# Optimization experiments

Hardware: AMD Instinct MI355X
Metric: run time of the kernel (lower is better)

Reference implementation:

```python
import jax, jax.numpy as jnp
import numpy as np

B, S, H = 32, 2048, 1024

def setup_inputs() -> dict:
    key = jax.random.key(0)
    k1, k2, k3, k4, k5 = jax.random.split(key, 5)
    sc = 1.0 / np.sqrt(2 * H)
    return {
        "hidden": jax.random.normal(k1, (B, H), dtype=jnp.float32),
        "encoder_outputs": jax.random.normal(k2, (B, S, H), dtype=jnp.float32),
        "W_attn": jax.random.normal(k3, (2 * H, H), dtype=jnp.float32) * sc,
        "b_attn": jax.random.normal(k4, (H,), dtype=jnp.float32) * sc,
        "v": jax.random.normal(k5, (H,), dtype=jnp.float32) * (1.0 / np.sqrt(H)),
    }

def reference(hidden, encoder_outputs, W_attn, b_attn, v):
    # Split W_attn into hidden-part and encoder-part instead of materializing
    # the (B,S,2H) concat: cat([h, enc]) @ W == h @ W[:H] + enc @ W[H:]
    Wh, We = W_attn[:H], W_attn[H:]                       # (H,H) each
    h_proj = hidden @ Wh + b_attn                          # (B, H)
    e_proj = jnp.einsum('bsh,hk->bsk', encoder_outputs, We)  # (B, S, H)
    energy = jnp.tanh(h_proj[:, None, :] + e_proj)         # (B, S, H)
    attention = jnp.einsum('bsh,h->bs', energy, v)         # (B, S)
    return jax.nn.softmax(attention, axis=1)
```

## Files before the change

### kernel.cpp

```cpp
#include <hip/hip_runtime.h>
#include <hip/hip_bf16.h>

#define H 1024
#define SEQ 2048
#define BATCH 32
#define MTOT (BATCH * SEQ)

#define BM 128
#define BN 128
#define BK 64

typedef __attribute__((ext_vector_type(4))) float f32x4;
typedef __attribute__((ext_vector_type(8))) __bf16 bf16x8;
typedef __attribute__((ext_vector_type(8))) unsigned short ushort8;

__device__ __forceinline__ unsigned short f2bf(float x) {
  __hip_bfloat16 h = __float2bfloat16(x);
  return __builtin_bit_cast(unsigned short, h);
}

__device__ __forceinline__ void gload_lds16(const void* g, void* l) {
  __builtin_amdgcn_global_load_lds(
      (const __attribute__((address_space(1))) unsigned int*)g,
      (__attribute__((address_space(3))) unsigned int*)l, 16, 0, 0);
}

__global__ void we_transpose_kernel(const float* __restrict__ W,
                                    unsigned short* __restrict__ WeT) {
  __shared__ float t[64][65];
  const int bn = blockIdx.x * 64;
  const int bk = blockIdx.y * 64;
  const int tid = threadIdx.x;
  const int ln = tid & 63;
  const int lk = tid >> 6;
  const float* src = W + (size_t)(H + bk) * H + bn;
#pragma unroll
  for (int i = 0; i < 16; ++i) {
    int k = i * 4 + lk;
    t[k][ln] = src[(size_t)k * H + ln];
  }
  __syncthreads();
  const int n = tid >> 2;
  const int kg = tid & 3;
  ushort8 o0, o1;
#pragma unroll
  for (int j = 0; j < 8; ++j) o0[j] = f2bf(t[kg * 16 + j][n]);
#pragma unroll
  for (int j = 0; j < 8; ++j) o1[j] = f2bf(t[kg * 16 + 8 + j][n]);
  unsigned short* dst = WeT + (size_t)(bn + n) * H + bk + kg * 16;
  *(ushort8*)(dst) = o0;
  *(ushort8*)(dst + 8) = o1;
}

__global__ void hproj_kernel(const float* __restrict__ hidden,
                             const float* __restrict__ W,
                             const float* __restrict__ b_attn,
                             float* __restrict__ hproj) {
  __shared__ float h[H];
  const int b = blockIdx.y;
  const int n = blockIdx.x * 256 + threadIdx.x;
  for (int i = threadIdx.x; i < H; i += 256) h[i] = hidden[(size_t)b * H + i];
  __syncthreads();
  float acc = b_attn[n];
#pragma unroll 8
  for (int k = 0; k < H; ++k) acc = fmaf(h[k], W[(size_t)k * H + n], acc);
  hproj[(size_t)b * H + n] = acc;
}

__global__ __launch_bounds__(256) void gemm_fused_kernel(
    const float* __restrict__ A,
    const unsigned short* __restrict__ WeT,
    const float* __restrict__ hproj,
    const float* __restrict__ v,
    float* __restrict__ partials)
{
  __shared__ __align__(16) unsigned short As[BM * BK];
  __shared__ __align__(16) unsigned short Bs[BN * BK];
  __shared__ float red[2][BM];

  const int bid = blockIdx.x;
  const int nb = bid & 7;
  const int mt = bid >> 3;
  const int m0 = mt * BM;
  const int bb = m0 / SEQ;

  const int tid = threadIdx.x;
  const int lane = tid & 63;
  const int w = tid >> 6;
  const int wm = w >> 1;
  const int wn = w & 1;

  const int a_c = tid & 15;
  const int a_r0 = tid >> 4;
  const float* a_src = A + (size_t)(m0 + a_r0) * H + a_c * 4;
  char* AsB = (char*)As;
  char* BsB = (char*)Bs;

  const char* b_src[4];
  char* b_dst[4];
#pragma unroll
  for (int i = 0; i < 4; ++i) {
    int q = (w * 4 + i) * 64 + lane;
    int nl = q >> 3;
    int c = (q & 7) ^ (nl & 7);
    b_src[i] = (const char*)WeT + ((size_t)(nb * 128 + nl) * H + c * 8) * 2;
    b_dst[i] = BsB + (w * 4 + i) * 1024;
  }

  f32x4 acc[4][4] = {};

  for (int ks = 0; ks < H / BK; ++ks) {
#pragma unroll
    for (int i = 0; i < 4; ++i) gload_lds16(b_src[i] + ks * 128, b_dst[i]);
#pragma unroll
    for (int p = 0; p < 8; ++p) {
      const int row = a_r0 + p * 16;
      f32x4 f = *(const f32x4*)(a_src + (size_t)p * 16 * H + ks * 64);
      unsigned int lo = f2bf(f[0]) | ((unsigned int)f2bf(f[1]) << 16);
      unsigned int hi = f2bf(f[2]) | ((unsigned int)f2bf(f[3]) << 16);
      int boff = (row * 128 + a_c * 8) ^ ((row & 7) << 4);
      *(uint2*)(AsB + boff) = make_uint2(lo, hi);
    }
    __syncthreads();

    bf16x8 af[4][2], bfr[4][2];
#pragma unroll
    for (int mi = 0; mi < 4; ++mi)
#pragma unroll
      for (int kk = 0; kk < 2; ++kk) {
        int row = wm * 64 + mi * 16 + (lane & 15);
        int c = kk * 4 + (lane >> 4);
        int off = (row * 128 + c * 16) ^ ((row & 7) << 4);
        af[mi][kk] = *(const bf16x8*)(AsB + off);
      }
#pragma unroll
    for (int ni = 0; ni < 4; ++ni)
#pragma unroll
      for (int kk = 0; kk < 2; ++kk) {
        int nl = wn * 64 + ni * 16 + (lane & 15);
        int c = kk * 4 + (lane >> 4);
        int off = (nl * 128 + c * 16) ^ ((nl & 7) << 4);
        bfr[ni][kk] = *(const bf16x8*)(BsB + off);
      }
#pragma unroll
    for (int kk = 0; kk < 2; ++kk)
#pragma unroll
      for (int mi = 0; mi < 4; ++mi)
#pragma unroll
        for (int ni = 0; ni < 4; ++ni)
          acc[mi][ni] = __builtin_amdgcn_mfma_f32_16x16x32_bf16(
              af[mi][kk], bfr[ni][kk], acc[mi][ni], 0, 0, 0);
    __syncthreads();
  }

  float rowsum[4][4];
#pragma unroll
  for (int mi = 0; mi < 4; ++mi)
#pragma unroll
    for (int i = 0; i < 4; ++i) rowsum[mi][i] = 0.f;

  const int colb = nb * 128 + wn * 64;
#pragma unroll
  for (int ni = 0; ni < 4; ++ni) {
    int colg = colb + ni * 16 + (lane & 15);
    float hp = hproj[(size_t)bb * H + colg];
    float vv = v[colg];
#pragma unroll
    for (int mi = 0; mi < 4; ++mi)
#pragma unroll
      for (int i = 0; i < 4; ++i)
        rowsum[mi][i] += tanhf(acc[mi][ni][i] + hp) * vv;
  }
#pragma unroll
  for (int mask = 1; mask <= 8; mask <<= 1)
#pragma unroll
    for (int mi = 0; mi < 4; ++mi)
#pragma unroll
      for (int i = 0; i < 4; ++i)
        rowsum[mi][i] += __shfl_xor(rowsum[mi][i], mask, 64);

  if ((lane & 15) == 0) {
    int rg = lane >> 4;
#pragma unroll
    for (int mi = 0; mi < 4; ++mi)
#pragma unroll
      for (int i = 0; i < 4; ++i)
        red[wn][wm * 64 + mi * 16 + rg * 4 + i] = rowsum[mi][i];
  }
  __syncthreads();
  if (tid < BM)
    partials[(size_t)nb * MTOT + m0 + tid] = red[0][tid] + red[1][tid];
}

__global__ void softmax_kernel(const float* __restrict__ partials,
                               float* __restrict__ out) {
  const int b = blockIdx.x;
  const int tid = threadIdx.x;
  const int ln = tid & 63;
  const int wid = tid >> 6;
  __shared__ float r1[4], r2[4];
  float loc[8];
  float lmax = -3.4e38f;
#pragma unroll
  for (int j = 0; j < 8; ++j) {
    int s = j * 256 + tid;
    float acc = 0.f;
#pragma unroll
    for (int p = 0; p < 8; ++p)
      acc += partials[(size_t)p * MTOT + (size_t)b * SEQ + s];
    loc[j] = acc;
    lmax = fmaxf(lmax, acc);
  }
#pragma unroll
  for (int m = 1; m <= 32; m <<= 1) lmax = fmaxf(lmax, __shfl_xor(lmax, m, 64));
  if (ln == 0) r1[wid] = lmax;
  __syncthreads();
  const float gmax = fmaxf(fmaxf(r1[0], r1[1]), fmaxf(r1[2], r1[3]));
  float lsum = 0.f;
#pragma unroll
  for (int j = 0; j < 8; ++j) {
    loc[j] = expf(loc[j] - gmax);
    lsum += loc[j];
  }
#pragma unroll
  for (int m = 1; m <= 32; m <<= 1) lsum += __shfl_xor(lsum, m, 64);
  if (ln == 0) r2[wid] = lsum;
  __syncthreads();
  const float inv = 1.f / (r2[0] + r2[1] + r2[2] + r2[3]);
#pragma unroll
  for (int j = 0; j < 8; ++j)
    out[(size_t)b * SEQ + j * 256 + tid] = loc[j] * inv;
}

extern "C" void kernel_launch(void* const* d_in, const int* in_sizes, int n_in,
                              void* d_out, int out_size, void* d_ws, size_t ws_size,
                              hipStream_t stream) {
  const float* hidden = (const float*)d_in[0];
  const float* enc    = (const float*)d_in[1];
  const float* W      = (const float*)d_in[2];
  const float* b_attn = (const float*)d_in[3];
  const float* v      = (const float*)d_in[4];
  float* out = (float*)d_out;

  char* ws = (char*)d_ws;
  unsigned short* WeT = (unsigned short*)ws;
  float* hproj    = (float*)(ws + (2u << 20));
  float* partials = (float*)(ws + (2u << 20) + (128u << 10));

  we_transpose_kernel<<<dim3(16, 16), 256, 0, stream>>>(W, WeT);
  hproj_kernel<<<dim3(4, BATCH), 256, 0, stream>>>(hidden, W, b_attn, hproj);
  gemm_fused_kernel<<<dim3(4096), 256, 0, stream>>>(enc, WeT, hproj, v, partials);
  softmax_kernel<<<dim3(BATCH), 256, 0, stream>>>(partials, out);
}
```

Measured before the change: 695.4 us.

## Double-buffer GEMM LDS tiles with register prefetch and remap blocks per XCD

```diff
diff --git a/kernel.cpp b/kernel.cpp
--- a/kernel.cpp
+++ b/kernel.cpp
@@ -9,6 +9,8 @@
 #define BM 128
 #define BN 128
 #define BK 64
+#define KSTEPS (H / BK)
+#define BUFB (BM * BK * 2)
 
 typedef __attribute__((ext_vector_type(4))) float f32x4;
 typedef __attribute__((ext_vector_type(8))) __bf16 bf16x8;
@@ -74,13 +76,15 @@
     const float* __restrict__ v,
     float* __restrict__ partials)
 {
-  __shared__ __align__(16) unsigned short As[BM * BK];
-  __shared__ __align__(16) unsigned short Bs[BN * BK];
+  __shared__ __align__(16) unsigned short As[2][BM * BK];
+  __shared__ __align__(16) unsigned short Bs[2][BN * BK];
   __shared__ float red[2][BM];
 
-  const int bid = blockIdx.x;
-  const int nb = bid & 7;
-  const int mt = bid >> 3;
+  const int d = blockIdx.x;
+  const int x = d & 7;
+  const int ii = d >> 3;
+  const int nb = ii & 7;
+  const int mt = x * 64 + (ii >> 3);
   const int m0 = mt * BM;
   const int bb = m0 / SEQ;
 
@@ -95,33 +99,50 @@
   const float* a_src = A + (size_t)(m0 + a_r0) * H + a_c * 4;
   char* AsB = (char*)As;
   char* BsB = (char*)Bs;
-
-  const char* b_src[4];
-  char* b_dst[4];
+  const int a_boff = (a_r0 * 128 + a_c * 8) ^ ((a_r0 & 7) << 4);
+
+  const char* bsrc[4];
+  int bdst[4];
 #pragma unroll
   for (int i = 0; i < 4; ++i) {
     int q = (w * 4 + i) * 64 + lane;
     int nl = q >> 3;
     int c = (q & 7) ^ (nl & 7);
-    b_src[i] = (const char*)WeT + ((size_t)(nb * 128 + nl) * H + c * 8) * 2;
-    b_dst[i] = BsB + (w * 4 + i) * 1024;
+    bsrc[i] = (const char*)WeT + ((size_t)(nb * 128 + nl) * H + c * 8) * 2;
+    bdst[i] = (w * 4 + i) * 1024;
   }
 
   f32x4 acc[4][4] = {};
 
-  for (int ks = 0; ks < H / BK; ++ks) {
-#pragma unroll
-    for (int i = 0; i < 4; ++i) gload_lds16(b_src[i] + ks * 128, b_dst[i]);
-#pragma unroll
-    for (int p = 0; p < 8; ++p) {
-      const int row = a_r0 + p * 16;
-      f32x4 f = *(const f32x4*)(a_src + (size_t)p * 16 * H + ks * 64);
-      unsigned int lo = f2bf(f[0]) | ((unsigned int)f2bf(f[1]) << 16);
-      unsigned int hi = f2bf(f[2]) | ((unsigned int)f2bf(f[3]) << 16);
-      int boff = (row * 128 + a_c * 8) ^ ((row & 7) << 4);
-      *(uint2*)(AsB + boff) = make_uint2(lo, hi);
+#pragma unroll
+  for (int i = 0; i < 4; ++i) gload_lds16(bsrc[i], BsB + bdst[i]);
+#pragma unroll
+  for (int p = 0; p < 8; ++p) {
+    f32x4 f = *(const f32x4*)(a_src + (size_t)p * 16 * H);
+    unsigned int lo = f2bf(f[0]) | ((unsigned int)f2bf(f[1]) << 16);
+    unsigned int hi = f2bf(f[2]) | ((unsigned int)f2bf(f[3]) << 16);
+    *(uint2*)(AsB + ((a_boff + p * 16 * 128) ^ 0)) = make_uint2(lo, hi);
+  }
+  __syncthreads();
+
+#pragma unroll 2
+  for (int ks = 0; ks < KSTEPS; ++ks) {
+    const int cur = ks & 1;
+    char* curA = AsB + cur * BUFB;
+    char* curB = BsB + cur * BUFB;
+    char* nxtA = AsB + (cur ^ 1) * BUFB;
+    char* nxtB = BsB + (cur ^ 1) * BUFB;
+    const bool pf = (ks + 1) < KSTEPS;
+
+    f32x4 fa[8];
+    if (pf) {
+#pragma unroll
+      for (int p = 0; p < 8; ++p)
+        fa[p] = *(const f32x4*)(a_src + (size_t)p * 16 * H + (ks + 1) * 64);
+#pragma unroll
+      for (int i = 0; i < 4; ++i)
+        gload_lds16(bsrc[i] + (size_t)(ks + 1) * 128, nxtB + bdst[i]);
     }
-    __syncthreads();
 
     bf16x8 af[4][2], bfr[4][2];
 #pragma unroll
@@ -131,7 +152,7 @@
         int row = wm * 64 + mi * 16 + (lane & 15);
         int c = kk * 4 + (lane >> 4);
         int off = (row * 128 + c * 16) ^ ((row & 7) << 4);
-        af[mi][kk] = *(const bf16x8*)(AsB + off);
+        af[mi][kk] = *(const bf16x8*)(curA + off);
       }
 #pragma unroll
     for (int ni = 0; ni < 4; ++ni)
@@ -140,8 +161,20 @@
         int nl = wn * 64 + ni * 16 + (lane & 15);
         int c = kk * 4 + (lane >> 4);
         int off = (nl * 128 + c * 16) ^ ((nl & 7) << 4);
-        bfr[ni][kk] = *(const bf16x8*)(BsB + off);
+        bfr[ni][kk] = *(const bf16x8*)(curB + off);
       }
+
+    if (pf) {
+#pragma unroll
+      for (int p = 0; p < 8; ++p) {
+        unsigned int lo = f2bf(fa[p][0]) | ((unsigned int)f2bf(fa[p][1]) << 16);
+        unsigned int hi = f2bf(fa[p][2]) | ((unsigned int)f2bf(fa[p][3]) << 16);
+        int row = a_r0 + p * 16;
+        int boff = (row * 128 + a_c * 8) ^ ((row & 7) << 4);
+        *(uint2*)(nxtA + boff) = make_uint2(lo, hi);
+      }
+    }
+
 #pragma unroll
     for (int kk = 0; kk < 2; ++kk)
 #pragma unroll
```

Result: faster. 678.1 us (-2.5%).
